# Optimization experiments

Hardware: AMD Instinct MI355X
Metric: run time of the kernel (lower is better)

The kernel has to match this reference:

```python
import jax, jax.numpy as jnp
import numpy as np

NEG_BIG = -9e15  # matches -9000000000000000.0 in the torch source
ALPHA = 0.2      # LeakyReLU negative slope


def setup_inputs() -> dict:
    key = jax.random.key(0)
    k1, k2, k3, k4 = jax.random.split(key, 4)
    N, F_in, F_out = 8192, 256, 128
    x = jax.random.normal(k1, (N, F_in), dtype=jnp.float32)
    adj = jax.random.randint(k2, (N, N), 0, 2, dtype=jnp.int32)
    W = jax.random.normal(k3, (F_in, F_out), dtype=jnp.float32) * 0.05
    a = jax.random.normal(k4, (2 * F_out, 1), dtype=jnp.float32) * 0.05
    return {"x": x, "adj": adj, "W": W, "a": a}


def reference(x, adj, W, a):
    # h = x @ W : [N, F]
    h = x @ W
    F_out = W.shape[1]
    # Algebraically identical to the concat formulation:
    # a^T [h_i || h_j] = h_i @ a1 + h_j @ a2
    a1 = a[:F_out, 0]
    a2 = a[F_out:, 0]
    src = h @ a1  # [N]
    dst = h @ a2  # [N]
    e = jax.nn.leaky_relu(src[:, None] + dst[None, :], negative_slope=ALPHA)  # [N, N]
    attention = jnp.where(adj > 0, e, NEG_BIG)
    attention = jax.nn.softmax(attention, axis=1)
    # dropout is identity in eval mode (training=False)
    h_prime = attention @ h  # [N, F]
    return h_prime
```

## Files before the change

kernel.cpp:

```cpp
#include <hip/hip_runtime.h>
#include <cstdint>

#define N 8192
#define FIN 256
#define FOUT 128
#define ALPHA 0.2f
#define JP 4
#define JSL (N / JP)
#define TJ 64
#define NTILE (JSL / TJ)
#define RB 32
#define SST 72

typedef unsigned short u16;
typedef __attribute__((ext_vector_type(8))) short short8;
typedef __attribute__((ext_vector_type(4))) float floatx4;

__device__ __forceinline__ u16 bf16_rne(float f) {
  uint32_t u = __float_as_uint(f);
  u += 0x7fff + ((u >> 16) & 1);
  return (u16)(u >> 16);
}

__device__ __forceinline__ void gl_lds16(const void* g, void* l) {
  __builtin_amdgcn_global_load_lds(
      (const __attribute__((address_space(1))) void*)g,
      (__attribute__((address_space(3))) void*)l, 16, 0, 0);
}

__global__ __launch_bounds__(256) void k_proj(const float* __restrict__ x,
                                              const float* __restrict__ W,
                                              const float* __restrict__ a,
                                              u16* __restrict__ hT3,
                                              float* __restrict__ srcv,
                                              float* __restrict__ dstv) {
  __shared__ float xs[8 * FIN];
  __shared__ float partS[4][4], partD[4][4];
  const int t = threadIdx.x;
  const int R0 = blockIdx.x * 8;

  const float4* xv = (const float4*)(x + (size_t)R0 * FIN);
  float4* xsv = (float4*)xs;
  xsv[t] = xv[t];
  xsv[t + 256] = xv[t + 256];
  __syncthreads();

  const int c  = t & 127;
  const int rg = (t >> 7) * 4;

  float acc[4] = {0.f, 0.f, 0.f, 0.f};
  float wa[4], wb[4];
  #pragma unroll
  for (int j = 0; j < 4; ++j) wa[j] = W[j * FOUT + c];
  #pragma unroll
  for (int j = 0; j < 4; ++j) wb[j] = W[(4 + j) * FOUT + c];

  for (int k4 = 0; k4 < FIN / 4; ++k4) {
    float wc[4];
    #pragma unroll
    for (int j = 0; j < 4; ++j) { wc[j] = wa[j]; wa[j] = wb[j]; }
    const int kn = (k4 + 2 < FIN / 4) ? k4 + 2 : k4;
    #pragma unroll
    for (int j = 0; j < 4; ++j) wb[j] = W[(kn * 4 + j) * FOUT + c];
    #pragma unroll
    for (int i = 0; i < 4; ++i) {
      const float4 xq = *(const float4*)&xs[(rg + i) * FIN + k4 * 4];
      acc[i] += xq.x * wc[0] + xq.y * wc[1] + xq.z * wc[2] + xq.w * wc[3];
    }
  }

  {
    const int j = R0 + rg;
    const int jb = j >> 5, q = (j >> 3) & 3, jj = j & 7;
    const int m = c & 15, nt = c >> 4;
    union { u16 u[4]; uint2 v; } pk;
    #pragma unroll
    for (int i = 0; i < 4; ++i) pk.u[i] = bf16_rne(acc[i]);
    *(uint2*)(hT3 + (size_t)(((jb * 8 + nt) * 64) + (m * 4 + q)) * 8 + jj) = pk.v;
  }

  const float a1 = a[c], a2 = a[FOUT + c];
  float s4[4], d4[4];
  #pragma unroll
  for (int i = 0; i < 4; ++i) { s4[i] = acc[i] * a1; d4[i] = acc[i] * a2; }
  #pragma unroll
  for (int off = 32; off > 0; off >>= 1) {
    #pragma unroll
    for (int i = 0; i < 4; ++i) {
      s4[i] += __shfl_down(s4[i], off);
      d4[i] += __shfl_down(d4[i], off);
    }
  }
  const int wv = t >> 6, lane = t & 63;
  if (lane == 0) {
    #pragma unroll
    for (int i = 0; i < 4; ++i) { partS[wv][i] = s4[i]; partD[wv][i] = d4[i]; }
  }
  __syncthreads();
  if (t < 16) {
    const int i = t & 3, rg2 = (t >> 2) & 1, which = t >> 3;
    if (which == 0) srcv[R0 + rg2 * 4 + i] = partS[rg2*2][i] + partS[rg2*2+1][i];
    else            dstv[R0 + rg2 * 4 + i] = partD[rg2*2][i] + partD[rg2*2+1][i];
  }
}

__global__ __launch_bounds__(256, 4) void k_gat(const int* __restrict__ adj,
                                                const u16* __restrict__ hT3,
                                                const float* __restrict__ srcv,
                                                const float* __restrict__ dstv,
                                                float* __restrict__ P,
                                                float* __restrict__ lp) {
  __shared__ u16 hS[2][8192];
  __shared__ u16 S[RB * SST];
  const int t = threadIdx.x;
  const int wv = t >> 6, lane = t & 63;
  const int q = lane >> 4, m = lane & 15;
  const int bm = blockIdx.x & 255;
  const int jp = blockIdx.x >> 8;
  const int R0 = bm * RB;
  const int j0 = jp * JSL;

  const int pr = t >> 3;
  const int pc = (t & 7) * 8;
  const float srcr = srcv[R0 + pr];
  const int*   adjp = adj + (size_t)(R0 + pr) * N + j0 + pc;
  const float* dstp = dstv + j0 + pc;

  const int rh = wv & 1, ch = wv >> 1;
  const int Lq = m * 4 + q;

  floatx4 acc[4];
  #pragma unroll
  for (int nt = 0; nt < 4; ++nt) acc[nt] = (floatx4){0.f, 0.f, 0.f, 0.f};
  float lsum = 0.f;

  const size_t jb00 = (size_t)(j0 >> 5);
  #define STAGE(I, BUF)                                                        \
  {                                                                            \
    _Pragma("unroll")                                                          \
    for (int cc = 0; cc < 4; ++cc) {                                           \
      const int kc = wv * 4 + cc;                                   \
      const int jbl = kc >> 3, nt_ = kc & 7;                                   \
      const u16* src = hT3 + ((jb00 + (size_t)(I) * 2 + jbl) * 8 + nt_) * 512  \
                       + (size_t)lane * 8;                                     \
      gl_lds16(src, &hS[BUF][kc * 512]);                                       \
    }                                                                          \
  }

  STAGE(0, 0)
  int4   aC0 = *(const int4*)(adjp),     aC1 = *(const int4*)(adjp + 4);
  float4 dC0 = *(const float4*)(dstp),   dC1 = *(const float4*)(dstp + 4);

  int buf = 0;
  for (int i = 0; i < NTILE; ++i) {
    __syncthreads();

    const int nx = (i + 1 < NTILE) ? i + 1 : i;
    if (i + 1 < NTILE) STAGE(i + 1, buf ^ 1)
    int4   aN0 = *(const int4*)(adjp + nx * TJ);
    int4   aN1 = *(const int4*)(adjp + nx * TJ + 4);
    float4 dN0 = *(const float4*)(dstp + nx * TJ);
    float4 dN1 = *(const float4*)(dstp + nx * TJ + 4);

    {
      const int   ai[8] = {aC0.x, aC0.y, aC0.z, aC0.w, aC1.x, aC1.y, aC1.z, aC1.w};
      const float df[8] = {dC0.x, dC0.y, dC0.z, dC0.w, dC1.x, dC1.y, dC1.z, dC1.w};
      union { u16 u[8]; short8 s; } pk;
      #pragma unroll
      for (int e = 0; e < 8; ++e) {
        float v = srcr + df[e];
        v = fmaxf(v, ALPHA * v);
        const float p = ai[e] > 0 ? __expf(v) : 0.f;
        lsum += p;
        pk.u[e] = bf16_rne(p);
      }
      *(short8*)&S[pr * SST + pc] = pk.s;
    }

    __syncthreads();

    {
      const short8 a0 = *(const short8*)&S[(rh * 16 + m) * SST + q * 8];
      const short8 a1 = *(const short8*)&S[(rh * 16 + m) * SST + 32 + q * 8];
      #pragma unroll
      for (int nt = 0; nt < 4; ++nt) {
        const short8 b0 = *(const short8*)&hS[buf][(0 * 8 + ch * 4 + nt) * 512 + Lq * 8];
        const short8 b1 = *(const short8*)&hS[buf][(1 * 8 + ch * 4 + nt) * 512 + Lq * 8];
        acc[nt] = __builtin_amdgcn_mfma_f32_16x16x32_bf16(a0, b0, acc[nt], 0, 0, 0);
        acc[nt] = __builtin_amdgcn_mfma_f32_16x16x32_bf16(a1, b1, acc[nt], 0, 0, 0);
      }
    }

    aC0 = aN0; aC1 = aN1; dC0 = dN0; dC1 = dN1;
    buf ^= 1;
  }
  #undef STAGE

  lsum += __shfl_down(lsum, 4);
  lsum += __shfl_down(lsum, 2);
  lsum += __shfl_down(lsum, 1);
  if ((t & 7) == 0) lp[(size_t)jp * N + R0 + pr] = lsum;

  float* Pp = P + ((size_t)jp * N + R0 + rh * 16) * FOUT + ch * 64;
  #pragma unroll
  for (int nt = 0; nt < 4; ++nt)
    #pragma unroll
    for (int ri = 0; ri < 4; ++ri)
      Pp[(size_t)(q * 4 + ri) * FOUT + nt * 16 + m] = acc[nt][ri];
}

__global__ __launch_bounds__(256) void k_norm(const float* __restrict__ P,
                                              const float* __restrict__ lp,
                                              float* __restrict__ out) {
  const int idx = blockIdx.x * 256 + threadIdx.x;
  const int rr = idx >> 5;
  const int c4 = (idx & 31) * 4;
  float l = 0.f;
  #pragma unroll
  for (int j = 0; j < JP; ++j) l += lp[j * N + rr];
  const float inv = 1.0f / l;
  float4 s = {0.f, 0.f, 0.f, 0.f};
  #pragma unroll
  for (int j = 0; j < JP; ++j) {
    const float4 p = *(const float4*)(P + ((size_t)j * N + rr) * FOUT + c4);
    s.x += p.x; s.y += p.y; s.z += p.z; s.w += p.w;
  }
  s.x *= inv; s.y *= inv; s.z *= inv; s.w *= inv;
  *(float4*)(out + (size_t)rr * FOUT + c4) = s;
}

extern "C" void kernel_launch(void* const* d_in, const int* in_sizes, int n_in,
                              void* d_out, int out_size, void* d_ws, size_t ws_size,
                              hipStream_t stream) {
  const float* x   = (const float*)d_in[0];
  const int*   adj = (const int*)d_in[1];
  const float* W   = (const float*)d_in[2];
  const float* a   = (const float*)d_in[3];
  float* out = (float*)d_out;

  char* ws = (char*)d_ws;
  u16*   hT3  = (u16*)ws;     ws += (size_t)FOUT * N * sizeof(u16);
  float* srcv = (float*)ws;   ws += (size_t)N * sizeof(float);
  float* dstv = (float*)ws;   ws += (size_t)N * sizeof(float);
  float* P    = (float*)ws;   ws += (size_t)JP * N * FOUT * sizeof(float);
  float* lp   = (float*)ws;   ws += (size_t)JP * N * sizeof(float);

  k_proj<<<N / 8, 256, 0, stream>>>(x, W, a, hT3, srcv, dstv);
  k_gat <<<256 * JP, 256, 0, stream>>>(adj, hT3, srcv, dstv, P, lp);
  k_norm<<<(N * FOUT / 4) / 256, 256, 0, stream>>>(P, lp, out);
}
```

Measured before the change: 432.6 us.

## Pack adjacency into bitmask and build MFMA A-fragments in registers

A pre-pass fused into the projection kernel packs the int32 adjacency matrix into a 1-bit-per-entry mask. The attention kernel then reads 8 MB of mask bytes instead of streaming the int32 adjacency inside its MFMA loop. Each wave now builds its bf16 probability fragments directly in registers, which removes the LDS staging buffer and one barrier per tile. The loop is also manually unrolled by two, with explicit waitcnt and sched_barrier pipelining. The cost is an extra full pass over adj, and the exp work is duplicated across the two column-half waves.

```diff
diff --git a/kernel.cpp b/kernel.cpp
--- a/kernel.cpp
+++ b/kernel.cpp
@@ -10,9 +10,10 @@
 #define TJ 64
 #define NTILE (JSL / TJ)
 #define RB 32
-#define SST 72
+#define PACKB (N * N / 32 / 256)
 
 typedef unsigned short u16;
+typedef unsigned char u8;
 typedef __attribute__((ext_vector_type(8))) short short8;
 typedef __attribute__((ext_vector_type(4))) float floatx4;
 
@@ -28,7 +29,9 @@
       (__attribute__((address_space(3))) void*)l, 16, 0, 0);
 }
 
-__global__ __launch_bounds__(256) void k_proj(const float* __restrict__ x,
+__global__ __launch_bounds__(256) void k_prep(const int* __restrict__ adj,
+                                              uint32_t* __restrict__ bmo,
+                                              const float* __restrict__ x,
                                               const float* __restrict__ W,
                                               const float* __restrict__ a,
                                               u16* __restrict__ hT3,
@@ -36,8 +39,28 @@
                                               float* __restrict__ dstv) {
   __shared__ float xs[8 * FIN];
   __shared__ float partS[4][4], partD[4][4];
+  const int bid = blockIdx.x;
   const int t = threadIdx.x;
-  const int R0 = blockIdx.x * 8;
+
+  if (bid < PACKB) {
+    const int tt = bid * 256 + t;
+    const int4* p = (const int4*)adj + (size_t)tt * 8;
+    int4 v[8];
+    #pragma unroll
+    for (int k = 0; k < 8; ++k) v[k] = p[k];
+    uint32_t mk = 0;
+    #pragma unroll
+    for (int k = 0; k < 8; ++k) {
+      mk |= (uint32_t)(v[k].x > 0) << (4 * k + 0);
+      mk |= (uint32_t)(v[k].y > 0) << (4 * k + 1);
+      mk |= (uint32_t)(v[k].z > 0) << (4 * k + 2);
+      mk |= (uint32_t)(v[k].w > 0) << (4 * k + 3);
+    }
+    bmo[tt] = mk;
+    return;
+  }
+
+  const int R0 = (bid - PACKB) * 8;
 
   const float4* xv = (const float4*)(x + (size_t)R0 * FIN);
   float4* xsv = (float4*)xs;
@@ -104,14 +127,13 @@
   }
 }
 
-__global__ __launch_bounds__(256, 4) void k_gat(const int* __restrict__ adj,
+__global__ __launch_bounds__(256, 4) void k_gat(const u8* __restrict__ bmk,
                                                 const u16* __restrict__ hT3,
                                                 const float* __restrict__ srcv,
                                                 const float* __restrict__ dstv,
                                                 float* __restrict__ P,
                                                 float* __restrict__ lp) {
   __shared__ u16 hS[2][8192];
-  __shared__ u16 S[RB * SST];
   const int t = threadIdx.x;
   const int wv = t >> 6, lane = t & 63;
   const int q = lane >> 4, m = lane & 15;
@@ -120,14 +142,13 @@
   const int R0 = bm * RB;
   const int j0 = jp * JSL;
 
-  const int pr = t >> 3;
-  const int pc = (t & 7) * 8;
-  const float srcr = srcv[R0 + pr];
-  const int*   adjp = adj + (size_t)(R0 + pr) * N + j0 + pc;
-  const float* dstp = dstv + j0 + pc;
-
   const int rh = wv & 1, ch = wv >> 1;
   const int Lq = m * 4 + q;
+
+  const int row = R0 + rh * 16 + m;
+  const float srcr = srcv[row];
+  const float* dstp = dstv + j0 + q * 8;
+  const u8*    bmp  = bmk + (size_t)row * (N >> 3) + (j0 >> 3) + q;
 
   floatx4 acc[4];
   #pragma unroll
@@ -147,59 +168,103 @@
     }                                                                          \
   }
 
+  #define GBODY(i, BUF, dA, dB, mA, mB, dAn, dBn, mAn, mBn)                    \
+  {                                                                            \
+    asm volatile("s_waitcnt vmcnt(4) lgkmcnt(0)" ::: "memory");                \
+    __builtin_amdgcn_s_barrier();                                              \
+    __builtin_amdgcn_sched_barrier(0);                                         \
+    if ((i) + 1 < NTILE) STAGE((i) + 1, (BUF) ^ 1)                             \
+    __builtin_amdgcn_sched_barrier(0);     \
+    const int nx_ = ((i) + 1 < NTILE) ? (i) + 1 : (i);                         \
+    dAn = *(const float4*)(dstp + nx_ * TJ);                                   \
+    dBn = *(const float4*)(dstp + nx_ * TJ + 32);                              \
+    mAn = bmp[nx_ * 8];                                                        \
+    mBn = bmp[nx_ * 8 + 4];                                                    \
+    union { u16 u[8]; short8 s; } A0_, A1_;                                    \
+    {                                                                          \
+      const float dfa[8] = {dA.x, dA.y, dA.z, dA.w, dA.x, dA.y, dA.z, dA.w};   \
+      (void)dfa;                                \
+    }                                                                          \
+    {                                                                          \
+      const float f0[4] = {dA.x, dA.y, dA.z, dA.w};                            \
+      _Pragma("unroll")                                                        \
+      for (int e = 0; e < 4; ++e) {                                            \
+        float v = srcr + f0[e];                                                \
+        v = fmaxf(v, ALPHA * v);                                               \
+        const float p = ((mA >> e) & 1) ? __expf(v) : 0.f;                     \
+        lsum += p; A0_.u[e] = bf16_rne(p);                                     \
+      }                                                                        \
+      const float f1[4] = {dA.w, dA.w, dA.w, dA.w};                            \
+      (void)f1;                                                                \
+    }                                                                          \
+    GBODY_UNUSED                                                               \
+  }
+
+  #undef GBODY
+  #undef GBODY_UNUSED
+
+  auto mk_frag = [&](const float4 dlo, const float4 dhi, const u8 mk,
+                     float& ls) -> short8 {
+    union { u16 u[8]; short8 s; } A_;
+    const float df[8] = {dlo.x, dlo.y, dlo.z, dlo.w, dhi.x, dhi.y, dhi.z, dhi.w};
+    #pragma unroll
+    for (int e = 0; e < 8; ++e) {
+      float v = srcr + df[e];
+      v = fmaxf(v, ALPHA * v);
+      const float p = ((mk >> e) & 1) ? __expf(v) : 0.f;
+      ls += p;
+      A_.u[e] = bf16_rne(p);
+    }
+    return A_.s;
+  };
+
+  #define GSTAGE(i, BUF, dA0, dA1, dB0, dB1, mA, mB,                           \
+                        dC0, dC1, dD0, dD1, mC, mD)                            \
+  {                                                                            \
+    asm volatile("s_waitcnt vmcnt(4) lgkmcnt(0)" ::: "memory");                \
+    __builtin_amdgcn_s_barrier();                                              \
+    __builtin_amdgcn_sched_barrier(0);                                         \
+    if ((i) + 1 < NTILE) STAGE((i) + 1, (BUF) ^ 1)                             \
+    __builtin_amdgcn_sched_barrier(0);     \
+    const int nx_ = ((i) + 1 < NTILE) ? (i) + 1 : (i);                         \
+    dC0 = *(const float4*)(dstp + nx_ * TJ);                                   \
+    dC1 = *(const float4*)(dstp + nx_ * TJ + 4);                               \
+    dD0 = *(const float4*)(dstp + nx_ * TJ + 32);                              \
+    dD1 = *(const float4*)(dstp + nx_ * TJ + 36);                              \
+    mC = bmp[nx_ * 8];                                                         \
+    mD = bmp[nx_ * 8 + 4];                                                     \
+    const short8 a0 = mk_frag(dA0, dA1, mA, lsum);                             \
+    const short8 a1 = mk_frag(dB0, dB1, mB, lsum);                             \
+    _Pragma("unroll")                                                          \
+    for (int nt = 0; nt < 4; ++nt) {                                           \
+      const short8 b0 = *(const short8*)&hS[BUF][(0 * 8 + ch * 4 + nt) * 512 + Lq * 8]; \
+      const short8 b1 = *(const short8*)&hS[BUF][(1 * 8 + ch * 4 + nt) * 512 + Lq * 8]; \
+      acc[nt] = __builtin_amdgcn_mfma_f32_16x16x32_bf16(a0, b0, acc[nt], 0, 0, 0); \
+      acc[nt] = __builtin_amdgcn_mfma_f32_16x16x32_bf16(a1, b1, acc[nt], 0, 0, 0); \
+    }                                                                          \
+  }
+
   STAGE(0, 0)
-  int4   aC0 = *(const int4*)(adjp),     aC1 = *(const int4*)(adjp + 4);
-  float4 dC0 = *(const float4*)(dstp),   dC1 = *(const float4*)(dstp + 4);
-
-  int buf = 0;
-  for (int i = 0; i < NTILE; ++i) {
-    __syncthreads();
-
-    const int nx = (i + 1 < NTILE) ? i + 1 : i;
-    if (i + 1 < NTILE) STAGE(i + 1, buf ^ 1)
-    int4   aN0 = *(const int4*)(adjp + nx * TJ);
-    int4   aN1 = *(const int4*)(adjp + nx * TJ + 4);
-    float4 dN0 = *(const float4*)(dstp + nx * TJ);
-    float4 dN1 = *(const float4*)(dstp + nx * TJ + 4);
-
-    {
-      const int   ai[8] = {aC0.x, aC0.y, aC0.z, aC0.w, aC1.x, aC1.y, aC1.z, aC1.w};
-      const float df[8] = {dC0.x, dC0.y, dC0.z, dC0.w, dC1.x, dC1.y, dC1.z, dC1.w};
-      union { u16 u[8]; short8 s; } pk;
-      #pragma unroll
-      for (int e = 0; e < 8; ++e) {
-        float v = srcr + df[e];
-        v = fmaxf(v, ALPHA * v);
-        const float p = ai[e] > 0 ? __expf(v) : 0.f;
-        lsum += p;
-        pk.u[e] = bf16_rne(p);
-      }
-      *(short8*)&S[pr * SST + pc] = pk.s;
-    }
-
-    __syncthreads();
-
-    {
-      const short8 a0 = *(const short8*)&S[(rh * 16 + m) * SST + q * 8];
-      const short8 a1 = *(const short8*)&S[(rh * 16 + m) * SST + 32 + q * 8];
-      #pragma unroll
-      for (int nt = 0; nt < 4; ++nt) {
-        const short8 b0 = *(const short8*)&hS[buf][(0 * 8 + ch * 4 + nt) * 512 + Lq * 8];
-        const short8 b1 = *(const short8*)&hS[buf][(1 * 8 + ch * 4 + nt) * 512 + Lq * 8];
-        acc[nt] = __builtin_amdgcn_mfma_f32_16x16x32_bf16(a0, b0, acc[nt], 0, 0, 0);
-        acc[nt] = __builtin_amdgcn_mfma_f32_16x16x32_bf16(a1, b1, acc[nt], 0, 0, 0);
-      }
-    }
-
-    aC0 = aN0; aC1 = aN1; dC0 = dN0; dC1 = dN1;
-    buf ^= 1;
-  }
+  __builtin_amdgcn_sched_barrier(0);
+  float4 pA0 = *(const float4*)(dstp);
+  float4 pA1 = *(const float4*)(dstp + 4);
+  float4 pB0 = *(const float4*)(dstp + 32);
+  float4 pB1 = *(const float4*)(dstp + 36);
+  u8 pmA = bmp[0], pmB = bmp[4];
+  float4 qA0, qA1, qB0, qB1; u8 qmA, qmB;
+
+  for (int i = 0; i < NTILE; i += 2) {
+    GSTAGE(i,     0, pA0, pA1, pB0, pB1, pmA, pmB,
+                     qA0, qA1, qB0, qB1, qmA, qmB)
+    GSTAGE(i + 1, 1, qA0, qA1, qB0, qB1, qmA, qmB,
+                     pA0, pA1, pB0, pB1, pmA, pmB)
+  }
+  #undef GSTAGE
   #undef STAGE
 
-  lsum += __shfl_down(lsum, 4);
-  lsum += __shfl_down(lsum, 2);
-  lsum += __shfl_down(lsum, 1);
-  if ((t & 7) == 0) lp[(size_t)jp * N + R0 + pr] = lsum;
+  lsum += __shfl_xor(lsum, 16);
+  lsum += __shfl_xor(lsum, 32);
+  if (ch == 0 && q == 0) lp[(size_t)jp * N + row] = lsum;
 
   float* Pp = P + ((size_t)jp * N + R0 + rh * 16) * FOUT + ch * 64;
   #pragma unroll
@@ -244,8 +309,10 @@
   float* dstv = (float*)ws;   ws += (size_t)N * sizeof(float);
   float* P    = (float*)ws;   ws += (size_t)JP * N * FOUT * sizeof(float);
   float* lp   = (float*)ws;   ws += (size_t)JP * N * sizeof(float);
-
-  k_proj<<<N / 8, 256, 0, stream>>>(x, W, a, hT3, srcv, dstv);
-  k_gat <<<256 * JP, 256, 0, stream>>>(adj, hT3, srcv, dstv, P, lp);
+  u8*    bmk  = (u8*)ws;      ws += (size_t)N * (N / 8);
+
+  k_prep<<<PACKB + N / 8, 256, 0, stream>>>(adj, (uint32_t*)bmk, x, W, a,
+                                            hT3, srcv, dstv);
+  k_gat <<<256 * JP, 256, 0, stream>>>(bmk, hT3, srcv, dstv, P, lp);
   k_norm<<<(N * FOUT / 4) / 256, 256, 0, stream>>>(P, lp, out);
 }
```

After: 461.1 us. 1.07x slower.
